# Performance work log

Hardware: AMD Instinct MI355X
Metric: run time of the kernel (lower is better)

The kernel has to match this reference:

```python
import jax, jax.numpy as jnp
import numpy as np

SEQ_LS = [512, 512, 512, 512]
HEADS = 8
DIM_HEAD = 64
DIM = 512
INNER = HEADS * DIM_HEAD  # 512
N = sum(SEQ_LS)           # 2048
B = 4
EPS = 1e-5

# static modality id per token position: [N]
MOD_IDS = jnp.asarray(np.repeat(np.arange(len(SEQ_LS)), SEQ_LS))


def setup_inputs() -> dict:
    key = jax.random.key(0)
    ks = jax.random.split(key, 6)
    x = jax.random.normal(ks[0], (B, N, DIM), dtype=jnp.float32)
    m_labels = jnp.ones((B, len(SEQ_LS)), dtype=jnp.int64 if jax.config.jax_enable_x64 else jnp.int32)
    gamma = jnp.ones((DIM,), dtype=jnp.float32)
    beta = jnp.zeros((DIM,), dtype=jnp.float32)
    w_qkv = jax.random.normal(ks[1], (DIM, 3 * INNER), dtype=jnp.float32) * (DIM ** -0.5)
    w_out = jax.random.normal(ks[2], (INNER, DIM), dtype=jnp.float32) * (INNER ** -0.5)
    b_out = jnp.zeros((DIM,), dtype=jnp.float32)
    return {"x": x, "m_labels": m_labels, "gamma": gamma, "beta": beta,
            "w_qkv": w_qkv, "w_out": w_out, "b_out": b_out}


def _additive_mask(m_labels):
    # present[b, n] = modality of token n is present in sample b
    present = (m_labels[:, MOD_IDS] != 0)                       # [B, N] bool
    pair_ok = present[:, :, None] & present[:, None, :]         # [B, N, N]
    neg_inf = jnp.float32(-jnp.inf)
    return jnp.where(pair_ok, jnp.float32(0.0), neg_inf)        # [B, N, N]


def reference(x, m_labels, gamma, beta, w_qkv, w_out, b_out):
    # LayerNorm(dim)
    mu = jnp.mean(x, axis=-1, keepdims=True)
    var = jnp.mean(jnp.square(x - mu), axis=-1, keepdims=True)
    xn = (x - mu) * jax.lax.rsqrt(var + EPS) * gamma + beta

    # QKV projection (no bias), split heads
    qkv = jnp.einsum('bnd,de->bne', xn, w_qkv)                  # [B, N, 3*INNER]
    q, k, v = jnp.split(qkv, 3, axis=-1)
    def heads(t):
        return t.reshape(B, N, HEADS, DIM_HEAD).transpose(0, 2, 1, 3)  # [B, H, N, Dh]
    q, k, v = heads(q), heads(k), heads(v)

    scale = DIM_HEAD ** -0.5
    dots = jnp.einsum('bhnd,bhmd->bhnm', q, k) * scale          # [B, H, N, N]
    dots = dots + _additive_mask(m_labels)[:, None, :, :]
    attn = jax.nn.softmax(dots, axis=-1)
    out = jnp.einsum('bhnm,bhmd->bhnd', attn, v)                # [B, H, N, Dh]
    out = out.transpose(0, 2, 1, 3).reshape(B, N, INNER)        # [B, N, INNER]
    return jnp.einsum('bni,io->bno', out, w_out) + b_out        # [B, N, DIM]
```

## Files before the change

kernel.cpp:

```cpp
#include <hip/hip_runtime.h>

#define DIMD 512
#define NTOK 2048
#define HEADS 8
#define DH 64

typedef __attribute__((ext_vector_type(4))) float f32x4;
typedef __attribute__((ext_vector_type(8))) __bf16 bf16x8;
typedef __attribute__((ext_vector_type(4))) short s16x4;

#define MFMA16(a, b, c) __builtin_amdgcn_mfma_f32_16x16x32_bf16((a), (b), (c), 0, 0, 0)
#define MFMAK16(a, b, c) __builtin_amdgcn_mfma_f32_16x16x16bf16_1k((a), (b), (c), 0, 0, 0)

__device__ __forceinline__ unsigned short f2bf(float f) {
  unsigned int u = __float_as_uint(f);
  u += 0x7fffu + ((u >> 16) & 1u);
  return (unsigned short)(u >> 16);
}

__device__ __forceinline__ float fexp2(float x) {
  float r;
  asm("v_exp_f32 %0, %1" : "=v"(r) : "v"(x));
  return r;
}

__device__ __forceinline__ unsigned packhi(float b, float a) {
#if __has_builtin(__builtin_amdgcn_perm)
  return __builtin_amdgcn_perm(__float_as_uint(a), __float_as_uint(b), 0x07060302u);
#else
  return (__float_as_uint(b) >> 16) | (__float_as_uint(a) & 0xffff0000u);
#endif
}

__device__ __forceinline__ void gl2lds16(const void* g, void* l) {
  auto gp = reinterpret_cast<__attribute__((address_space(1))) unsigned int*>(
      reinterpret_cast<unsigned long long>(g));
  auto lp = reinterpret_cast<__attribute__((address_space(3))) unsigned int*>(
      reinterpret_cast<unsigned long long>(l));
  __builtin_amdgcn_global_load_lds(gp, lp, 16, 0, 0);
}

__global__ __launch_bounds__(256) void prep_kernel(const float* __restrict__ x,
                                                   const float* __restrict__ gamma,
                                                   const float* __restrict__ beta,
                                                   const float* __restrict__ w_qkv,
                                                   const float* __restrict__ w_out,
                                                   unsigned short* __restrict__ xn,
                                                   unsigned short* __restrict__ wqkvT,
                                                   unsigned short* __restrict__ woutT) {
  __shared__ float t[32][33];
  const int bid = blockIdx.x;
  if (bid < 2048) {
    const int row = bid * 4 + (threadIdx.x >> 6);
    const int lane = threadIdx.x & 63;
    const float4* xr = (const float4*)(x + (size_t)row * DIMD);
    float4 a = xr[lane];
    float4 b = xr[lane + 64];
    float s = a.x + a.y + a.z + a.w + b.x + b.y + b.z + b.w;
    for (int off = 1; off < 64; off <<= 1) s += __shfl_xor(s, off, 64);
    float mu = s * (1.0f / DIMD);
    float d0 = a.x - mu, d1 = a.y - mu, d2 = a.z - mu, d3 = a.w - mu;
    float e0 = b.x - mu, e1 = b.y - mu, e2 = b.z - mu, e3 = b.w - mu;
    float v = d0 * d0 + d1 * d1 + d2 * d2 + d3 * d3 + e0 * e0 + e1 * e1 + e2 * e2 + e3 * e3;
    for (int off = 1; off < 64; off <<= 1) v += __shfl_xor(v, off, 64);
    float rs = rsqrtf(v * (1.0f / DIMD) + 1e-5f);
    const float4* g4 = (const float4*)gamma;
    const float4* be4 = (const float4*)beta;
    float4 ga = g4[lane], gb = g4[lane + 64];
    float4 ba = be4[lane], bb = be4[lane + 64];
    unsigned p0 = (unsigned)f2bf(d0 * rs * ga.x + ba.x) | ((unsigned)f2bf(d1 * rs * ga.y + ba.y) << 16);
    unsigned p1 = (unsigned)f2bf(d2 * rs * ga.z + ba.z) | ((unsigned)f2bf(d3 * rs * ga.w + ba.w) << 16);
    unsigned p2 = (unsigned)f2bf(e0 * rs * gb.x + bb.x) | ((unsigned)f2bf(e1 * rs * gb.y + bb.y) << 16);
    unsigned p3 = (unsigned)f2bf(e2 * rs * gb.z + bb.z) | ((unsigned)f2bf(e3 * rs * gb.w + bb.w) << 16);
    uint2 w0; w0.x = p0; w0.y = p1;
    uint2 w1; w1.x = p2; w1.y = p3;
    *(uint2*)&xn[(size_t)row * DIMD + lane * 4] = w0;
    *(uint2*)&xn[(size_t)row * DIMD + 256 + lane * 4] = w1;
  } else {
    const float* w;
    unsigned short* wt;
    int C, bx, by;
    if (bid < 2816) { w = w_qkv; wt = wqkvT; C = 1536; bx = (bid - 2048) % 48; by = (bid - 2048) / 48; }
    else            { w = w_out; wt = woutT; C = 512;  bx = (bid - 2816) % 16; by = (bid - 2816) / 16; }
    const int R = 512;
    int tx = threadIdx.x & 31, ty = threadIdx.x >> 5;
    int c0 = bx * 32, r0 = by * 32;
    for (int i = 0; i < 4; i++)
      t[ty + 8 * i][tx] = w[(size_t)(r0 + ty + 8 * i) * C + c0 + tx];
    __syncthreads();
    for (int i = 0; i < 4; i++)
      wt[(size_t)(c0 + ty + 8 * i) * R + r0 + tx] = f2bf(t[tx][ty + 8 * i]);
  }
}

__global__ __launch_bounds__(256, 2) void qkv_gemm(const unsigned short* __restrict__ A,
                                                   const unsigned short* __restrict__ Bt,
                                                   unsigned short* __restrict__ qb,
                                                   unsigned short* __restrict__ kb,
                                                   unsigned short* __restrict__ vtb) {
  __shared__ unsigned short As[2][128 * 64];
  __shared__ unsigned short Bs[2][128 * 64];
  const int tid = threadIdx.x;
  const int wave = tid >> 6, lane = tid & 63;
  const int row16 = lane & 15, quad = lane >> 4;
  const int rho = row16 & 7;
  const int m0 = blockIdx.x * 128;
  const int n0 = blockIdx.y * 128;
  const int rw = (wave & 1) * 64, cw = (wave >> 1) * 64;

  const char* Ab = (const char*)A;
  const char* Bb = (const char*)Bt;
#pragma unroll
  for (int i = 0; i < 4; i++) {
    int idx = i * 256 + tid;
    int r = idx >> 3;
    int c = (idx & 7) ^ (r & 7);
    gl2lds16(Ab + ((size_t)(m0 + r) * DIMD) * 2 + c * 16, (char*)As[0] + idx * 16);
    gl2lds16(Bb + ((size_t)(n0 + r) * DIMD) * 2 + c * 16, (char*)Bs[0] + idx * 16);
  }
  __syncthreads();

  f32x4 acc[4][4] = {};
  for (int kt = 0; kt < 8; kt++) {
    const int buf = kt & 1;
    if (kt < 7) {
      const int k0 = (kt + 1) * 64;
#pragma unroll
      for (int i = 0; i < 4; i++) {
        int idx = i * 256 + tid;
        int r = idx >> 3;
        int c = (idx & 7) ^ (r & 7);
        gl2lds16(Ab + ((size_t)(m0 + r) * DIMD + k0) * 2 + c * 16, (char*)As[buf ^ 1] + idx * 16);
        gl2lds16(Bb + ((size_t)(n0 + r) * DIMD + k0) * 2 + c * 16, (char*)Bs[buf ^ 1] + idx * 16);
      }
    }
#pragma unroll
    for (int ks = 0; ks < 2; ks++) {
      bf16x8 av[4], bv[4];
#pragma unroll
      for (int i = 0; i < 4; i++) {
        int Ra = rw + i * 16 + row16;
        int Rb = cw + i * 16 + row16;
        av[i] = *(const bf16x8*)&As[buf][Ra * 64 + (((ks * 4 + quad) ^ rho) * 8)];
        bv[i] = *(const bf16x8*)&Bs[buf][Rb * 64 + (((ks * 4 + quad) ^ rho) * 8)];
      }
#pragma unroll
      for (int i = 0; i < 4; i++)
#pragma unroll
        for (int j = 0; j < 4; j++) acc[i][j] = MFMA16(av[i], bv[j], acc[i][j]);
    }
    __syncthreads();
  }

  unsigned short* Ct = (unsigned short*)As;
#pragma unroll
  for (int i = 0; i < 4; i++)
#pragma unroll
    for (int j = 0; j < 4; j++)
#pragma unroll
      for (int r = 0; r < 4; r++)
        Ct[(rw + i * 16 + quad * 4 + r) * 136 + cw + j * 16 + row16] = f2bf(acc[i][j][r]);
  __syncthreads();

  const int sect = n0 >> 9;
  const int h0 = (n0 & 511) >> 6;
  const int b = m0 >> 11;
  const int nbase = m0 & 2047;
  if (sect < 2) {
    unsigned short* dst = (sect == 0) ? qb : kb;
#pragma unroll
    for (int i = 0; i < 8; i++) {
      int cid = i * 256 + tid;
      int row = cid >> 4, col0 = (cid & 15) * 8;
      int h = h0 + (col0 >> 6), d0 = col0 & 63;
      uint4 val = *(const uint4*)&Ct[row * 136 + col0];
      *(uint4*)&dst[(((size_t)(b * HEADS + h) * NTOK) + nbase + row) * DH + d0] = val;
    }
  } else {
#pragma unroll
    for (int u = 0; u < 4; u++) {
      int uid = u * 256 + tid;
      int col = uid >> 3, rc = (uid & 7) * 16;
      int h = h0 + (col >> 6), d = col & 63;
      unsigned short tmp[16];
#pragma unroll
      for (int j = 0; j < 16; j++) tmp[j] = Ct[(rc + j) * 136 + col];
      size_t base = ((size_t)(b * HEADS + h) * DH + d) * NTOK + nbase + rc;
      *(uint4*)&vtb[base] = *(uint4*)&tmp[0];
      *(uint4*)&vtb[base + 8] = *(uint4*)&tmp[8];
    }
  }
}

__global__ __launch_bounds__(512) void attn_kernel(const unsigned short* __restrict__ qb,
                                                   const unsigned short* __restrict__ kb,
                                                   const unsigned short* __restrict__ vtb,
                                                   const int* __restrict__ mlab,
                                                   unsigned short* __restrict__ ao) {
  __shared__ unsigned short Qs[256 * 64];
  __shared__ unsigned short Ks[2][64 * 64];
  __shared__ unsigned short Vs[2][64 * 64];
  const int tid = threadIdx.x;
  const int wave = tid >> 6, lane = tid & 63;
  const int row16 = lane & 15, quad = lane >> 4;
  const int rho = row16 & 7;
  const int bh = blockIdx.x;
  const int b = bh >> 3, h = bh & 7;
  const int q0 = blockIdx.y * 256;

  const char* qg = (const char*)(qb + ((size_t)bh * NTOK + q0) * DH);
  const char* kgb = (const char*)(kb + (size_t)bh * NTOK * DH);
  const char* vgb = (const char*)(vtb + (size_t)bh * DH * NTOK);
  const int sr = tid >> 3;
  const int sc = (tid & 7) ^ (sr & 7);

#pragma unroll
  for (int i = 0; i < 4; i++)
    gl2lds16(qg + (sr + 64 * i) * 128 + sc * 16, (char*)Qs + tid * 16 + i * 8192);
  gl2lds16(kgb + sr * 128 + sc * 16, (char*)Ks[0] + tid * 16);
  gl2lds16(vgb + (size_t)sr * 4096 + sc * 16, (char*)Vs[0] + tid * 16);
  __syncthreads();

  bf16x8 aq[2][2];
#pragma unroll
  for (int qs = 0; qs < 2; qs++) {
    const int qrow = wave * 32 + qs * 16 + row16;
#pragma unroll
    for (int ki = 0; ki < 2; ki++)
      aq[qs][ki] = *(const bf16x8*)&Qs[qrow * 64 + (((ki * 4 + quad) ^ rho) * 8)];
  }

  f32x4 accT[4][2] = {};
  float lsum[2] = {0.f, 0.f};
  const float cs = 0.125f * 1.44269504088896f;
  const float c0 = mlab[b * 4 + 0] ? -16.f : -100000.f;
  const float c1 = mlab[b * 4 + 1] ? -16.f : -100000.f;
  const float c2 = mlab[b * 4 + 2] ? -16.f : -100000.f;
  const float c3 = mlab[b * 4 + 3] ? -16.f : -100000.f;

  for (int t = 0; t < 32; t++) {
    const int buf = t & 1;
    if (t < 31) {
      gl2lds16(kgb + (size_t)(t + 1) * 8192 + sr * 128 + sc * 16, (char*)Ks[buf ^ 1] + tid * 16);
      gl2lds16(vgb + (size_t)(t + 1) * 128 + (size_t)sr * 4096 + sc * 16, (char*)Vs[buf ^ 1] + tid * 16);
    }
    f32x4 S[2][4];
#pragma unroll
    for (int f = 0; f < 4; f++) {
      const unsigned short* Kr = &Ks[buf][(f * 16 + row16) * 64];
      bf16x8 ak0 = *(const bf16x8*)&Kr[(quad ^ rho) * 8];
      bf16x8 ak1 = *(const bf16x8*)&Kr[((quad + 4) ^ rho) * 8];
#pragma unroll
      for (int qs = 0; qs < 2; qs++) {
        f32x4 z = {};
        z = MFMA16(ak0, aq[qs][0], z);
        z = MFMA16(ak1, aq[qs][1], z);
        S[qs][f] = z;
      }
    }
    const int mi = t >> 3;
    const float c = (mi == 0) ? c0 : (mi == 1) ? c1 : (mi == 2) ? c2 : c3;
    s16x4 pf[2][4];
#pragma unroll
    for (int qs = 0; qs < 2; qs++)
#pragma unroll
      for (int f = 0; f < 4; f++) {
        float p0 = fexp2(fmaf(S[qs][f][0], cs, c));
        float p1 = fexp2(fmaf(S[qs][f][1], cs, c));
        float p2 = fexp2(fmaf(S[qs][f][2], cs, c));
        float p3 = fexp2(fmaf(S[qs][f][3], cs, c));
        lsum[qs] += (p0 + p1) + (p2 + p3);
        uint2 pk;
        pk.x = packhi(p0, p1);
        pk.y = packhi(p2, p3);
        pf[qs][f] = *(s16x4*)&pk;
      }
#pragma unroll
    for (int g = 0; g < 4; g++) {
      const unsigned short* Vr = &Vs[buf][(g * 16 + row16) * 64];
#pragma unroll
      for (int u = 0; u < 4; u++) {
        s16x4 va = *(const s16x4*)&Vr[(((2 * u + (quad >> 1)) ^ rho) * 8) + (quad & 1) * 4];
#pragma unroll
        for (int qs = 0; qs < 2; qs++) accT[g][qs] = MFMAK16(va, pf[qs][u], accT[g][qs]);
      }
    }
    __syncthreads();
  }

#pragma unroll
  for (int qs = 0; qs < 2; qs++) {
    float s = lsum[qs];
    s += __shfl_xor(s, 16, 64);
    s += __shfl_xor(s, 32, 64);
    lsum[qs] = 1.0f / s;
  }
#pragma unroll
  for (int qs = 0; qs < 2; qs++) {
    const int q = q0 + wave * 32 + qs * 16 + row16;
    unsigned short* aor = ao + ((size_t)b * NTOK + q) * DIMD + h * DH;
#pragma unroll
    for (int g = 0; g < 4; g++) {
      *(unsigned*)&aor[g * 16 + quad * 4] = packhi(accT[g][qs][0] * lsum[qs], accT[g][qs][1] * lsum[qs]);
      *(unsigned*)&aor[g * 16 + quad * 4 + 2] = packhi(accT[g][qs][2] * lsum[qs], accT[g][qs][3] * lsum[qs]);
    }
  }
}

__global__ __launch_bounds__(256, 2) void out_gemm(const unsigned short* __restrict__ A,
                                                   const unsigned short* __restrict__ Bt,
                                                   const float* __restrict__ bias,
                                                   float* __restrict__ out) {
  __shared__ unsigned short As[2][128 * 64];
  __shared__ unsigned short Bs[2][64 * 64];
  const int tid = threadIdx.x;
  const int wave = tid >> 6, lane = tid & 63;
  const int row16 = lane & 15, quad = lane >> 4;
  const int rho = row16 & 7;
  const int m0 = blockIdx.x * 128;
  const int n0 = blockIdx.y * 64;
  const int rw = (wave & 1) * 64, cw = (wave >> 1) * 32;

  const char* Ab = (const char*)A;
  const char* Bb = (const char*)Bt;
#pragma unroll
  for (int i = 0; i < 4; i++) {
    int idx = i * 256 + tid;
    int r = idx >> 3;
    int c = (idx & 7) ^ (r & 7);
    gl2lds16(Ab + ((size_t)(m0 + r) * DIMD) * 2 + c * 16, (char*)As[0] + idx * 16);
  }
#pragma unroll
  for (int i = 0; i < 2; i++) {
    int idx = i * 256 + tid;
    int r = idx >> 3;
    int c = (idx & 7) ^ (r & 7);
    gl2lds16(Bb + ((size_t)(n0 + r) * DIMD) * 2 + c * 16, (char*)Bs[0] + idx * 16);
  }
  __syncthreads();

  f32x4 acc[4][2] = {};
  for (int kt = 0; kt < 8; kt++) {
    const int buf = kt & 1;
    if (kt < 7) {
      const int k0 = (kt + 1) * 64;
#pragma unroll
      for (int i = 0; i < 4; i++) {
        int idx = i * 256 + tid;
        int r = idx >> 3;
        int c = (idx & 7) ^ (r & 7);
        gl2lds16(Ab + ((size_t)(m0 + r) * DIMD + k0) * 2 + c * 16, (char*)As[buf ^ 1] + idx * 16);
      }
#pragma unroll
      for (int i = 0; i < 2; i++) {
        int idx = i * 256 + tid;
        int r = idx >> 3;
        int c = (idx & 7) ^ (r & 7);
        gl2lds16(Bb + ((size_t)(n0 + r) * DIMD + k0) * 2 + c * 16, (char*)Bs[buf ^ 1] + idx * 16);
      }
    }
#pragma unroll
    for (int ks = 0; ks < 2; ks++) {
      bf16x8 av[4], bv[2];
#pragma unroll
      for (int i = 0; i < 4; i++)
        av[i] = *(const bf16x8*)&As[buf][(rw + i * 16 + row16) * 64 + (((ks * 4 + quad) ^ rho) * 8)];
#pragma unroll
      for (int j = 0; j < 2; j++)
        bv[j] = *(const bf16x8*)&Bs[buf][(cw + j * 16 + row16) * 64 + (((ks * 4 + quad) ^ rho) * 8)];
#pragma unroll
      for (int i = 0; i < 4; i++)
#pragma unroll
        for (int j = 0; j < 2; j++) acc[i][j] = MFMA16(av[i], bv[j], acc[i][j]);
    }
    __syncthreads();
  }

#pragma unroll
  for (int j = 0; j < 2; j++) {
    const int col = n0 + cw + j * 16 + row16;
    const float bv = bias[col];
#pragma unroll
    for (int i = 0; i < 4; i++)
#pragma unroll
      for (int r = 0; r < 4; r++) {
        const int row = m0 + rw + i * 16 + quad * 4 + r;
        out[(size_t)row * DIMD + col] = acc[i][j][r] + bv;
      }
  }
}

extern "C" void kernel_launch(void* const* d_in, const int* in_sizes, int n_in,
                              void* d_out, int out_size, void* d_ws, size_t ws_size,
                              hipStream_t stream) {
  const float* x = (const float*)d_in[0];
  const int* mlab = (const int*)d_in[1];
  const float* gamma = (const float*)d_in[2];
  const float* beta = (const float*)d_in[3];
  const float* w_qkv = (const float*)d_in[4];
  const float* w_out = (const float*)d_in[5];
  const float* b_out = (const float*)d_in[6];
  float* out = (float*)d_out;

  char* ws = (char*)d_ws;
  unsigned short* xn = (unsigned short*)(ws);
  unsigned short* wqkvT = (unsigned short*)(ws + 8388608);
  unsigned short* woutT = (unsigned short*)(ws + 9961472);
  unsigned short* qbuf = (unsigned short*)(ws + 10485760);
  unsigned short* kbuf = (unsigned short*)(ws + 18874368);
  unsigned short* vtbuf = (unsigned short*)(ws + 27262976);
  unsigned short* aobuf = (unsigned short*)(ws + 35651584);

  prep_kernel<<<3072, 256, 0, stream>>>(x, gamma, beta, w_qkv, w_out, xn, wqkvT, woutT);
  qkv_gemm<<<dim3(64, 12), 256, 0, stream>>>(xn, wqkvT, qbuf, kbuf, vtbuf);
  attn_kernel<<<dim3(32, 8), 512, 0, stream>>>(qbuf, kbuf, vtbuf, mlab, aobuf);
  out_gemm<<<dim3(64, 8), 256, 0, stream>>>(aobuf, woutT, b_out, out);
}
```

Measured before the change: 153.4 us.

## Split attention key tiles across wave pairs with LDS reduction

Doubles the attention block to 1024 threads: each pair of waves shares the same 32 query rows but handles half of every 64-key tile, so per-wave softmax and MFMA work per iteration is halved. Partial accumulators and row sums from the odd waves go through LDS and are added by the even waves before normalization and store. The K and V tile loads are split between the two thread halves. This adds latency-hiding waves per CU at the cost of a larger LDS footprint, an extra barrier and a reduction epilogue. The fixed softmax offset with no running max is kept as before.

```diff
diff --git a/kernel.cpp b/kernel.cpp
--- a/kernel.cpp
+++ b/kernel.cpp
@@ -192,18 +192,20 @@
   }
 }
 
-__global__ __launch_bounds__(512) void attn_kernel(const unsigned short* __restrict__ qb,
-                                                   const unsigned short* __restrict__ kb,
-                                                   const unsigned short* __restrict__ vtb,
-                                                   const int* __restrict__ mlab,
-                                                   unsigned short* __restrict__ ao) {
-  __shared__ unsigned short Qs[256 * 64];
-  __shared__ unsigned short Ks[2][64 * 64];
-  __shared__ unsigned short Vs[2][64 * 64];
+__global__ __launch_bounds__(1024, 4) void attn_kernel(const unsigned short* __restrict__ qb,
+                                                       const unsigned short* __restrict__ kb,
+                                                       const unsigned short* __restrict__ vtb,
+                                                       const int* __restrict__ mlab,
+                                                       unsigned short* __restrict__ ao) {
+  __shared__ char SMEM[66560];
+  unsigned short* Qs = (unsigned short*)SMEM;
+  unsigned short* KsB = (unsigned short*)(SMEM + 32768);
+  unsigned short* VsB = (unsigned short*)(SMEM + 49152);
   const int tid = threadIdx.x;
   const int wave = tid >> 6, lane = tid & 63;
   const int row16 = lane & 15, quad = lane >> 4;
   const int rho = row16 & 7;
+  const int kw = wave & 1, qw = wave >> 1;
   const int bh = blockIdx.x;
   const int b = bh >> 3, h = bh & 7;
   const int q0 = blockIdx.y * 256;
@@ -211,20 +213,29 @@
   const char* qg = (const char*)(qb + ((size_t)bh * NTOK + q0) * DH);
   const char* kgb = (const char*)(kb + (size_t)bh * NTOK * DH);
   const char* vgb = (const char*)(vtb + (size_t)bh * DH * NTOK);
-  const int sr = tid >> 3;
-  const int sc = (tid & 7) ^ (sr & 7);
-
-#pragma unroll
-  for (int i = 0; i < 4; i++)
-    gl2lds16(qg + (sr + 64 * i) * 128 + sc * 16, (char*)Qs + tid * 16 + i * 8192);
-  gl2lds16(kgb + sr * 128 + sc * 16, (char*)Ks[0] + tid * 16);
-  gl2lds16(vgb + (size_t)sr * 4096 + sc * 16, (char*)Vs[0] + tid * 16);
+
+  const int half = tid >> 9;
+  const int stid = tid & 511;
+  const int sr = stid >> 3;
+  const int sc = (stid & 7) ^ (sr & 7);
+
+#pragma unroll
+  for (int i = 0; i < 2; i++) {
+    int idx = i * 1024 + tid;
+    int r = idx >> 3;
+    int c = (idx & 7) ^ (r & 7);
+    gl2lds16(qg + r * 128 + c * 16, SMEM + idx * 16);
+  }
+  if (half == 0)
+    gl2lds16(kgb + sr * 128 + sc * 16, (char*)KsB + stid * 16);
+  else
+    gl2lds16(vgb + (size_t)sr * 4096 + sc * 16, (char*)VsB + stid * 16);
   __syncthreads();
 
   bf16x8 aq[2][2];
 #pragma unroll
   for (int qs = 0; qs < 2; qs++) {
-    const int qrow = wave * 32 + qs * 16 + row16;
+    const int qrow = qw * 32 + qs * 16 + row16;
 #pragma unroll
     for (int ki = 0; ki < 2; ki++)
       aq[qs][ki] = *(const bf16x8*)&Qs[qrow * 64 + (((ki * 4 + quad) ^ rho) * 8)];
@@ -241,13 +252,17 @@
   for (int t = 0; t < 32; t++) {
     const int buf = t & 1;
     if (t < 31) {
-      gl2lds16(kgb + (size_t)(t + 1) * 8192 + sr * 128 + sc * 16, (char*)Ks[buf ^ 1] + tid * 16);
-      gl2lds16(vgb + (size_t)(t + 1) * 128 + (size_t)sr * 4096 + sc * 16, (char*)Vs[buf ^ 1] + tid * 16);
-    }
-    f32x4 S[2][4];
-#pragma unroll
-    for (int f = 0; f < 4; f++) {
-      const unsigned short* Kr = &Ks[buf][(f * 16 + row16) * 64];
+      if (half == 0)
+        gl2lds16(kgb + (size_t)(t + 1) * 8192 + sr * 128 + sc * 16,
+                 (char*)KsB + (buf ^ 1) * 8192 + stid * 16);
+      else
+        gl2lds16(vgb + (size_t)(t + 1) * 128 + (size_t)sr * 4096 + sc * 16,
+                 (char*)VsB + (buf ^ 1) * 8192 + stid * 16);
+    }
+    f32x4 S[2][2];
+#pragma unroll
+    for (int f = 0; f < 2; f++) {
+      const unsigned short* Kr = KsB + buf * 4096 + (kw * 32 + f * 16 + row16) * 64;
       bf16x8 ak0 = *(const bf16x8*)&Kr[(quad ^ rho) * 8];
       bf16x8 ak1 = *(const bf16x8*)&Kr[((quad + 4) ^ rho) * 8];
 #pragma unroll
@@ -260,11 +275,11 @@
     }
     const int mi = t >> 3;
     const float c = (mi == 0) ? c0 : (mi == 1) ? c1 : (mi == 2) ? c2 : c3;
-    s16x4 pf[2][4];
+    s16x4 pf[2][2];
 #pragma unroll
     for (int qs = 0; qs < 2; qs++)
 #pragma unroll
-      for (int f = 0; f < 4; f++) {
+      for (int f = 0; f < 2; f++) {
         float p0 = fexp2(fmaf(S[qs][f][0], cs, c));
         float p1 = fexp2(fmaf(S[qs][f][1], cs, c));
         float p2 = fexp2(fmaf(S[qs][f][2], cs, c));
@@ -277,10 +292,10 @@
       }
 #pragma unroll
     for (int g = 0; g < 4; g++) {
-      const unsigned short* Vr = &Vs[buf][(g * 16 + row16) * 64];
-#pragma unroll
-      for (int u = 0; u < 4; u++) {
-        s16x4 va = *(const s16x4*)&Vr[(((2 * u + (quad >> 1)) ^ rho) * 8) + (quad & 1) * 4];
+      const unsigned short* Vr = VsB + buf * 4096 + (g * 16 + row16) * 64;
+#pragma unroll
+      for (int u = 0; u < 2; u++) {
+        s16x4 va = *(const s16x4*)&Vr[(((kw * 4 + 2 * u + (quad >> 1)) ^ rho) * 8) + (quad & 1) * 4];
 #pragma unroll
         for (int qs = 0; qs < 2; qs++) accT[g][qs] = MFMAK16(va, pf[qs][u], accT[g][qs]);
       }
@@ -293,16 +308,48 @@
     float s = lsum[qs];
     s += __shfl_xor(s, 16, 64);
     s += __shfl_xor(s, 32, 64);
-    lsum[qs] = 1.0f / s;
-  }
-#pragma unroll
-  for (int qs = 0; qs < 2; qs++) {
-    const int q = q0 + wave * 32 + qs * 16 + row16;
-    unsigned short* aor = ao + ((size_t)b * NTOK + q) * DIMD + h * DH;
-#pragma unroll
-    for (int g = 0; g < 4; g++) {
-      *(unsigned*)&aor[g * 16 + quad * 4] = packhi(accT[g][qs][0] * lsum[qs], accT[g][qs][1] * lsum[qs]);
-      *(unsigned*)&aor[g * 16 + quad * 4 + 2] = packhi(accT[g][qs][2] * lsum[qs], accT[g][qs][3] * lsum[qs]);
+    lsum[qs] = s;
+  }
+
+  float* Red = (float*)SMEM;
+  float* LRed = (float*)(SMEM + 65536);
+  if (kw) {
+    float* R = Red + qw * 2048;
+#pragma unroll
+    for (int g = 0; g < 4; g++)
+#pragma unroll
+      for (int qs = 0; qs < 2; qs++) {
+        int c2 = (g * 2 + qs) ^ (lane & 7);
+        *(f32x4*)&R[lane * 32 + c2 * 4] = accT[g][qs];
+      }
+    if (quad == 0)
+#pragma unroll
+      for (int qs = 0; qs < 2; qs++) LRed[qw * 32 + qs * 16 + row16] = lsum[qs];
+  }
+  __syncthreads();
+  if (kw == 0) {
+    float* R = Red + qw * 2048;
+#pragma unroll
+    for (int g = 0; g < 4; g++)
+#pragma unroll
+      for (int qs = 0; qs < 2; qs++) {
+        int c2 = (g * 2 + qs) ^ (lane & 7);
+        f32x4 o = *(const f32x4*)&R[lane * 32 + c2 * 4];
+        accT[g][qs] += o;
+      }
+    float inv[2];
+#pragma unroll
+    for (int qs = 0; qs < 2; qs++)
+      inv[qs] = 1.0f / (lsum[qs] + LRed[qw * 32 + qs * 16 + row16]);
+#pragma unroll
+    for (int qs = 0; qs < 2; qs++) {
+      const int q = q0 + qw * 32 + qs * 16 + row16;
+      unsigned short* aor = ao + ((size_t)b * NTOK + q) * DIMD + h * DH;
+#pragma unroll
+      for (int g = 0; g < 4; g++) {
+        *(unsigned*)&aor[g * 16 + quad * 4] = packhi(accT[g][qs][0] * inv[qs], accT[g][qs][1] * inv[qs]);
+        *(unsigned*)&aor[g * 16 + quad * 4 + 2] = packhi(accT[g][qs][2] * inv[qs], accT[g][qs][3] * inv[qs]);
+      }
     }
   }
 }
@@ -413,6 +460,6 @@
 
   prep_kernel<<<3072, 256, 0, stream>>>(x, gamma, beta, w_qkv, w_out, xn, wqkvT, woutT);
   qkv_gemm<<<dim3(64, 12), 256, 0, stream>>>(xn, wqkvT, qbuf, kbuf, vtbuf);
-  attn_kernel<<<dim3(32, 8), 512, 0, stream>>>(qbuf, kbuf, vtbuf, mlab, aobuf);
+  attn_kernel<<<dim3(32, 8), 1024, 0, stream>>>(qbuf, kbuf, vtbuf, mlab, aobuf);
   out_gemm<<<dim3(64, 8), 256, 0, stream>>>(aobuf, woutT, b_out, out);
 }
```

Result: no change. 153.7 us (+0.2%).

## Fuse all four stages into one cooperative persistent kernel with grid syncs

Applied to the files above, without the earlier changes.

Replaces the four launches (prep, QKV GEMM, attention, output GEMM) with one cooperative kernel of 256 blocks of 512 threads, separating the stages with grid.sync. Each stage is remapped onto the fixed grid, with two 256-thread sub-tiles per block for the GEMMs. This removes the launch gaps and per-kernel tail effects between stages. In exchange the stages run with lower parallelism than before (for example, fewer blocks for prep and the QKV GEMM) and pay the cost of the grid barriers. The old four-kernel path remains as a fallback if the cooperative launch fails.

```diff
diff --git a/kernel.cpp b/kernel.cpp
--- a/kernel.cpp
+++ b/kernel.cpp
@@ -1,4 +1,7 @@
 #include <hip/hip_runtime.h>
+#include <hip/hip_cooperative_groups.h>
+
+namespace cg = cooperative_groups;
 
 #define DIMD 512
 #define NTOK 2048
@@ -38,6 +41,376 @@
   auto lp = reinterpret_cast<__attribute__((address_space(3))) unsigned int*>(
       reinterpret_cast<unsigned long long>(l));
   __builtin_amdgcn_global_load_lds(gp, lp, 16, 0, 0);
+}
+
+__global__ __launch_bounds__(512, 2) void fused_all(
+    const float* __restrict__ x, const int* __restrict__ mlab,
+    const float* __restrict__ gamma, const float* __restrict__ beta,
+    const float* __restrict__ w_qkv, const float* __restrict__ w_out,
+    const float* __restrict__ b_out, float* __restrict__ out,
+    unsigned short* __restrict__ xn, unsigned short* __restrict__ wqkvT,
+    unsigned short* __restrict__ woutT, unsigned short* __restrict__ qb,
+    unsigned short* __restrict__ kb, unsigned short* __restrict__ vtb,
+    unsigned short* __restrict__ ao) {
+  __shared__ char SMEM[131072];
+  const int tid = threadIdx.x;
+  const int blk = blockIdx.x;
+  cg::grid_group grid = cg::this_grid();
+
+  {
+    const int wv = tid >> 6, lane = tid & 63;
+    const float4* g4 = (const float4*)gamma;
+    const float4* be4 = (const float4*)beta;
+    float4 ga = g4[lane], gb = g4[lane + 64];
+    float4 ba = be4[lane], bb = be4[lane + 64];
+#pragma unroll
+    for (int it = 0; it < 4; it++) {
+      const int row = it * 2048 + blk * 8 + wv;
+      const float4* xr = (const float4*)(x + (size_t)row * DIMD);
+      float4 a = xr[lane];
+      float4 b = xr[lane + 64];
+      float s = a.x + a.y + a.z + a.w + b.x + b.y + b.z + b.w;
+      for (int off = 1; off < 64; off <<= 1) s += __shfl_xor(s, off, 64);
+      float mu = s * (1.0f / DIMD);
+      float d0 = a.x - mu, d1 = a.y - mu, d2 = a.z - mu, d3 = a.w - mu;
+      float e0 = b.x - mu, e1 = b.y - mu, e2 = b.z - mu, e3 = b.w - mu;
+      float v = d0 * d0 + d1 * d1 + d2 * d2 + d3 * d3 + e0 * e0 + e1 * e1 + e2 * e2 + e3 * e3;
+      for (int off = 1; off < 64; off <<= 1) v += __shfl_xor(v, off, 64);
+      float rs = rsqrtf(v * (1.0f / DIMD) + 1e-5f);
+      unsigned p0 = (unsigned)f2bf(d0 * rs * ga.x + ba.x) | ((unsigned)f2bf(d1 * rs * ga.y + ba.y) << 16);
+      unsigned p1 = (unsigned)f2bf(d2 * rs * ga.z + ba.z) | ((unsigned)f2bf(d3 * rs * ga.w + ba.w) << 16);
+      unsigned p2 = (unsigned)f2bf(e0 * rs * gb.x + bb.x) | ((unsigned)f2bf(e1 * rs * gb.y + bb.y) << 16);
+      unsigned p3 = (unsigned)f2bf(e2 * rs * gb.z + bb.z) | ((unsigned)f2bf(e3 * rs * gb.w + bb.w) << 16);
+      uint2 w0; w0.x = p0; w0.y = p1;
+      uint2 w1; w1.x = p2; w1.y = p3;
+      *(uint2*)&xn[(size_t)row * DIMD + lane * 4] = w0;
+      *(uint2*)&xn[(size_t)row * DIMD + 256 + lane * 4] = w1;
+    }
+  }
+  {
+    const int sub = tid >> 8, stid = tid & 255;
+    float* t = (float*)(SMEM + sub * 4352);
+    const int tx = stid & 31, ty = stid >> 5;
+#pragma unroll
+    for (int it = 0; it < 2; it++) {
+      const int vb = it * 512 + blk * 2 + sub;
+      const float* w;
+      unsigned short* wt;
+      int C, bx, by;
+      if (vb < 768) { w = w_qkv; wt = wqkvT; C = 1536; bx = vb % 48; by = vb / 48; }
+      else          { int u2 = vb - 768; w = w_out; wt = woutT; C = 512; bx = u2 & 15; by = u2 >> 4; }
+      const int c0 = bx * 32, r0 = by * 32;
+      __syncthreads();
+      for (int i = 0; i < 4; i++)
+        t[(ty + 8 * i) * 33 + tx] = w[(size_t)(r0 + ty + 8 * i) * C + c0 + tx];
+      __syncthreads();
+      for (int i = 0; i < 4; i++)
+        wt[(size_t)(c0 + ty + 8 * i) * 512 + r0 + tx] = f2bf(t[tx * 33 + ty + 8 * i]);
+    }
+  }
+  __threadfence();
+  grid.sync();
+
+  {
+    const int h2 = tid >> 8, stid = tid & 255;
+    char* base = SMEM + h2 * 65536;
+    const int wv = stid >> 6, lane = stid & 63;
+    const int row16 = lane & 15, quad = lane >> 4;
+    const int rho = row16 & 7;
+    const int rw = (wv & 1) * 64, cw = (wv >> 1) * 64;
+    const char* Ab = (const char*)xn;
+    const char* Bb = (const char*)wqkvT;
+    unsigned short* AsF = (unsigned short*)base;
+    unsigned short* BsF = (unsigned short*)(base + 32768);
+#pragma unroll 1
+    for (int p = 0; p < 2; p++) {
+      const int v0 = p * 512 + blk * 2;
+      if (v0 < 768) {
+        const int v = v0 + h2;
+        const int m0 = (v & 63) * 128;
+        const int n0 = (v >> 6) * 128;
+#pragma unroll
+        for (int i = 0; i < 4; i++) {
+          int idx = i * 256 + stid;
+          int r = idx >> 3;
+          int c = (idx & 7) ^ (r & 7);
+          gl2lds16(Ab + ((size_t)(m0 + r) * DIMD) * 2 + c * 16, (char*)AsF + idx * 16);
+          gl2lds16(Bb + ((size_t)(n0 + r) * DIMD) * 2 + c * 16, (char*)BsF + idx * 16);
+        }
+        __syncthreads();
+        f32x4 acc[4][4] = {};
+        for (int kt = 0; kt < 8; kt++) {
+          const int buf = kt & 1;
+          if (kt < 7) {
+            const int k0 = (kt + 1) * 64;
+#pragma unroll
+            for (int i = 0; i < 4; i++) {
+              int idx = i * 256 + stid;
+              int r = idx >> 3;
+              int c = (idx & 7) ^ (r & 7);
+              gl2lds16(Ab + ((size_t)(m0 + r) * DIMD + k0) * 2 + c * 16,
+                       (char*)AsF + (buf ^ 1) * 16384 + idx * 16);
+              gl2lds16(Bb + ((size_t)(n0 + r) * DIMD + k0) * 2 + c * 16,
+                       (char*)BsF + (buf ^ 1) * 16384 + idx * 16);
+            }
+          }
+#pragma unroll
+          for (int ks = 0; ks < 2; ks++) {
+            bf16x8 av[4], bv[4];
+#pragma unroll
+            for (int i = 0; i < 4; i++) {
+              int Ra = rw + i * 16 + row16;
+              int Rb = cw + i * 16 + row16;
+              av[i] = *(const bf16x8*)&AsF[buf * 8192 + Ra * 64 + (((ks * 4 + quad) ^ rho) * 8)];
+              bv[i] = *(const bf16x8*)&BsF[buf * 8192 + Rb * 64 + (((ks * 4 + quad) ^ rho) * 8)];
+            }
+#pragma unroll
+            for (int i = 0; i < 4; i++)
+#pragma unroll
+              for (int j = 0; j < 4; j++) acc[i][j] = MFMA16(av[i], bv[j], acc[i][j]);
+          }
+          __syncthreads();
+        }
+        unsigned short* Ct = (unsigned short*)base;
+#pragma unroll
+        for (int i = 0; i < 4; i++)
+#pragma unroll
+          for (int j = 0; j < 4; j++)
+#pragma unroll
+            for (int r = 0; r < 4; r++)
+              Ct[(rw + i * 16 + quad * 4 + r) * 136 + cw + j * 16 + row16] = f2bf(acc[i][j][r]);
+        __syncthreads();
+        const int sect = n0 >> 9;
+        const int h0 = (n0 & 511) >> 6;
+        const int b = m0 >> 11;
+        const int nbase = m0 & 2047;
+        if (sect < 2) {
+          unsigned short* dst = (sect == 0) ? qb : kb;
+#pragma unroll
+          for (int i = 0; i < 8; i++) {
+            int cid = i * 256 + stid;
+            int row = cid >> 4, col0 = (cid & 15) * 8;
+            int hh = h0 + (col0 >> 6), d0 = col0 & 63;
+            uint4 val = *(const uint4*)&Ct[row * 136 + col0];
+            *(uint4*)&dst[(((size_t)(b * HEADS + hh) * NTOK) + nbase + row) * DH + d0] = val;
+          }
+        } else {
+#pragma unroll
+          for (int u = 0; u < 4; u++) {
+            int uid = u * 256 + stid;
+            int col = uid >> 3, rc = (uid & 7) * 16;
+            int hh = h0 + (col >> 6), d = col & 63;
+            unsigned short tmp[16];
+#pragma unroll
+            for (int j = 0; j < 16; j++) tmp[j] = Ct[(rc + j) * 136 + col];
+            size_t bq = ((size_t)(b * HEADS + hh) * DH + d) * NTOK + nbase + rc;
+            *(uint4*)&vtb[bq] = *(uint4*)&tmp[0];
+            *(uint4*)&vtb[bq + 8] = *(uint4*)&tmp[8];
+          }
+        }
+        __syncthreads();
+      }
+    }
+  }
+  __threadfence();
+  grid.sync();
+
+  {
+    unsigned short* Qs = (unsigned short*)SMEM;
+    unsigned short* Ks0 = (unsigned short*)(SMEM + 32768);
+    unsigned short* Vs0 = (unsigned short*)(SMEM + 49152);
+    const int wv = tid >> 6, lane = tid & 63;
+    const int row16 = lane & 15, quad = lane >> 4;
+    const int rho = row16 & 7;
+    const int bh = blk & 31;
+    const int b = bh >> 3, h = bh & 7;
+    const int q0 = (blk >> 5) * 256;
+
+    const char* qg = (const char*)(qb + ((size_t)bh * NTOK + q0) * DH);
+    const char* kgb = (const char*)(kb + (size_t)bh * NTOK * DH);
+    const char* vgb = (const char*)(vtb + (size_t)bh * DH * NTOK);
+    const int sr = tid >> 3;
+    const int sc = (tid & 7) ^ (sr & 7);
+
+#pragma unroll
+    for (int i = 0; i < 4; i++)
+      gl2lds16(qg + (sr + 64 * i) * 128 + sc * 16, (char*)Qs + tid * 16 + i * 8192);
+    gl2lds16(kgb + sr * 128 + sc * 16, (char*)Ks0 + tid * 16);
+    gl2lds16(vgb + (size_t)sr * 4096 + sc * 16, (char*)Vs0 + tid * 16);
+    __syncthreads();
+
+    bf16x8 aq[2][2];
+#pragma unroll
+    for (int qs = 0; qs < 2; qs++) {
+      const int qrow = wv * 32 + qs * 16 + row16;
+#pragma unroll
+      for (int ki = 0; ki < 2; ki++)
+        aq[qs][ki] = *(const bf16x8*)&Qs[qrow * 64 + (((ki * 4 + quad) ^ rho) * 8)];
+    }
+
+    f32x4 accT[4][2] = {};
+    float lsum[2] = {0.f, 0.f};
+    const float cs = 0.125f * 1.44269504088896f;
+    const float c0 = mlab[b * 4 + 0] ? -16.f : -100000.f;
+    const float c1 = mlab[b * 4 + 1] ? -16.f : -100000.f;
+    const float c2 = mlab[b * 4 + 2] ? -16.f : -100000.f;
+    const float c3 = mlab[b * 4 + 3] ? -16.f : -100000.f;
+
+    for (int t = 0; t < 32; t++) {
+      const int buf = t & 1;
+      if (t < 31) {
+        gl2lds16(kgb + (size_t)(t + 1) * 8192 + sr * 128 + sc * 16,
+                 (char*)Ks0 + (buf ^ 1) * 8192 + tid * 16);
+        gl2lds16(vgb + (size_t)(t + 1) * 128 + (size_t)sr * 4096 + sc * 16,
+                 (char*)Vs0 + (buf ^ 1) * 8192 + tid * 16);
+      }
+      f32x4 S[2][4];
+#pragma unroll
+      for (int f = 0; f < 4; f++) {
+        const unsigned short* Kr = Ks0 + buf * 4096 + (f * 16 + row16) * 64;
+        bf16x8 ak0 = *(const bf16x8*)&Kr[(quad ^ rho) * 8];
+        bf16x8 ak1 = *(const bf16x8*)&Kr[((quad + 4) ^ rho) * 8];
+#pragma unroll
+        for (int qs = 0; qs < 2; qs++) {
+          f32x4 z = {};
+          z = MFMA16(ak0, aq[qs][0], z);
+          z = MFMA16(ak1, aq[qs][1], z);
+          S[qs][f] = z;
+        }
+      }
+      const int mi = t >> 3;
+      const float c = (mi == 0) ? c0 : (mi == 1) ? c1 : (mi == 2) ? c2 : c3;
+      s16x4 pf[2][4];
+#pragma unroll
+      for (int qs = 0; qs < 2; qs++)
+#pragma unroll
+        for (int f = 0; f < 4; f++) {
+          float p0 = fexp2(fmaf(S[qs][f][0], cs, c));
+          float p1 = fexp2(fmaf(S[qs][f][1], cs, c));
+          float p2 = fexp2(fmaf(S[qs][f][2], cs, c));
+          float p3 = fexp2(fmaf(S[qs][f][3], cs, c));
+          lsum[qs] += (p0 + p1) + (p2 + p3);
+          uint2 pk;
+          pk.x = packhi(p0, p1);
+          pk.y = packhi(p2, p3);
+          pf[qs][f] = *(s16x4*)&pk;
+        }
+#pragma unroll
+      for (int g = 0; g < 4; g++) {
+        const unsigned short* Vr = Vs0 + buf * 4096 + (g * 16 + row16) * 64;
+#pragma unroll
+        for (int u = 0; u < 4; u++) {
+          s16x4 va = *(const s16x4*)&Vr[(((2 * u + (quad >> 1)) ^ rho) * 8) + (quad & 1) * 4];
+#pragma unroll
+          for (int qs = 0; qs < 2; qs++) accT[g][qs] = MFMAK16(va, pf[qs][u], accT[g][qs]);
+        }
+      }
+      __syncthreads();
+    }
+
+#pragma unroll
+    for (int qs = 0; qs < 2; qs++) {
+      float s = lsum[qs];
+      s += __shfl_xor(s, 16, 64);
+      s += __shfl_xor(s, 32, 64);
+      lsum[qs] = 1.0f / s;
+    }
+#pragma unroll
+    for (int qs = 0; qs < 2; qs++) {
+      const int q = q0 + wv * 32 + qs * 16 + row16;
+      unsigned short* aor = ao + ((size_t)b * NTOK + q) * DIMD + h * DH;
+#pragma unroll
+      for (int g = 0; g < 4; g++) {
+        *(unsigned*)&aor[g * 16 + quad * 4] = packhi(accT[g][qs][0] * lsum[qs], accT[g][qs][1] * lsum[qs]);
+        *(unsigned*)&aor[g * 16 + quad * 4 + 2] = packhi(accT[g][qs][2] * lsum[qs], accT[g][qs][3] * lsum[qs]);
+      }
+    }
+  }
+  __threadfence();
+  grid.sync();
+
+  {
+    const int h2 = tid >> 8, stid = tid & 255;
+    char* base = SMEM + h2 * 65536;
+    const int wv = stid >> 6, lane = stid & 63;
+    const int row16 = lane & 15, quad = lane >> 4;
+    const int rho = row16 & 7;
+    const int v = blk * 2 + h2;
+    const int m0 = (v & 63) * 128;
+    const int n0 = (v >> 6) * 64;
+    const int rw = (wv & 1) * 64, cw = (wv >> 1) * 32;
+    const char* Ab = (const char*)ao;
+    const char* Bb = (const char*)woutT;
+    unsigned short* AsF = (unsigned short*)base;
+    unsigned short* BsF = (unsigned short*)(base + 32768);
+#pragma unroll
+    for (int i = 0; i < 4; i++) {
+      int idx = i * 256 + stid;
+      int r = idx >> 3;
+      int c = (idx & 7) ^ (r & 7);
+      gl2lds16(Ab + ((size_t)(m0 + r) * DIMD) * 2 + c * 16, (char*)AsF + idx * 16);
+    }
+#pragma unroll
+    for (int i = 0; i < 2; i++) {
+      int idx = i * 256 + stid;
+      int r = idx >> 3;
+      int c = (idx & 7) ^ (r & 7);
+      gl2lds16(Bb + ((size_t)(n0 + r) * DIMD) * 2 + c * 16, (char*)BsF + idx * 16);
+    }
+    __syncthreads();
+
+    f32x4 acc[4][2] = {};
+    for (int kt = 0; kt < 8; kt++) {
+      const int buf = kt & 1;
+      if (kt < 7) {
+        const int k0 = (kt + 1) * 64;
+#pragma unroll
+        for (int i = 0; i < 4; i++) {
+          int idx = i * 256 + stid;
+          int r = idx >> 3;
+          int c = (idx & 7) ^ (r & 7);
+          gl2lds16(Ab + ((size_t)(m0 + r) * DIMD + k0) * 2 + c * 16,
+                   (char*)AsF + (buf ^ 1) * 16384 + idx * 16);
+        }
+#pragma unroll
+        for (int i = 0; i < 2; i++) {
+          int idx = i * 256 + stid;
+          int r = idx >> 3;
+          int c = (idx & 7) ^ (r & 7);
+          gl2lds16(Bb + ((size_t)(n0 + r) * DIMD + k0) * 2 + c * 16,
+                   (char*)BsF + (buf ^ 1) * 8192 + idx * 16);
+        }
+      }
+#pragma unroll
+      for (int ks = 0; ks < 2; ks++) {
+        bf16x8 av[4], bv[2];
+#pragma unroll
+        for (int i = 0; i < 4; i++)
+          av[i] = *(const bf16x8*)&AsF[buf * 8192 + (rw + i * 16 + row16) * 64 + (((ks * 4 + quad) ^ rho) * 8)];
+#pragma unroll
+        for (int j = 0; j < 2; j++)
+          bv[j] = *(const bf16x8*)&BsF[buf * 4096 + (cw + j * 16 + row16) * 64 + (((ks * 4 + quad) ^ rho) * 8)];
+#pragma unroll
+        for (int i = 0; i < 4; i++)
+#pragma unroll
+          for (int j = 0; j < 2; j++) acc[i][j] = MFMA16(av[i], bv[j], acc[i][j]);
+      }
+      __syncthreads();
+    }
+
+#pragma unroll
+    for (int j = 0; j < 2; j++) {
+      const int col = n0 + cw + j * 16 + row16;
+      const float bv = b_out[col];
+#pragma unroll
+      for (int i = 0; i < 4; i++)
+#pragma unroll
+        for (int r = 0; r < 4; r++) {
+          const int row = m0 + rw + i * 16 + quad * 4 + r;
+          out[(size_t)row * DIMD + col] = acc[i][j][r] + bv;
+        }
+    }
+  }
 }
 
 __global__ __launch_bounds__(256) void prep_kernel(const float* __restrict__ x,
@@ -411,8 +784,16 @@
   unsigned short* vtbuf = (unsigned short*)(ws + 27262976);
   unsigned short* aobuf = (unsigned short*)(ws + 35651584);
 
-  prep_kernel<<<3072, 256, 0, stream>>>(x, gamma, beta, w_qkv, w_out, xn, wqkvT, woutT);
-  qkv_gemm<<<dim3(64, 12), 256, 0, stream>>>(xn, wqkvT, qbuf, kbuf, vtbuf);
-  attn_kernel<<<dim3(32, 8), 512, 0, stream>>>(qbuf, kbuf, vtbuf, mlab, aobuf);
-  out_gemm<<<dim3(64, 8), 256, 0, stream>>>(aobuf, woutT, b_out, out);
-}
+  void* args[] = {(void*)&x,     (void*)&mlab,  (void*)&gamma, (void*)&beta,
+                  (void*)&w_qkv, (void*)&w_out, (void*)&b_out, (void*)&out,
+                  (void*)&xn,    (void*)&wqkvT, (void*)&woutT, (void*)&qbuf,
+                  (void*)&kbuf,  (void*)&vtbuf, (void*)&aobuf};
+  hipError_t e = hipLaunchCooperativeKernel((void*)fused_all, dim3(256), dim3(512),
+                                            args, 0, stream);
+  if (e != hipSuccess) {
+    prep_kernel<<<3072, 256, 0, stream>>>(x, gamma, beta, w_qkv, w_out, xn, wqkvT, woutT);
+    qkv_gemm<<<dim3(64, 12), 256, 0, stream>>>(xn, wqkvT, qbuf, kbuf, vtbuf);
+    attn_kernel<<<dim3(32, 8), 512, 0, stream>>>(qbuf, kbuf, vtbuf, mlab, aobuf);
+    out_gemm<<<dim3(64, 8), 256, 0, stream>>>(aobuf, woutT, b_out, out);
+  }
+}
```

Result: slower. 427.0 us (+178.3%).
